# Kernel tuning notes

Hardware: AMD Instinct MI355X
Metric: run time of the kernel (lower is better)

## Reference

```python
import jax, jax.numpy as jnp
import numpy as np

N = 50000    # nodes
E = 600000   # edges
H = 128      # hidden_dim
NF = 12      # n_features
L = 4        # n_layers
EPS = 1e-5   # LayerNorm eps


def setup_inputs() -> dict:
    key = jax.random.key(0)
    ks = jax.random.split(key, 32)

    def w(k, shape, fan_in):
        return (jax.random.normal(k, shape, jnp.float32) / np.float32(np.sqrt(fan_in)))

    inp = {
        "x": jax.random.normal(ks[0], (N, NF), jnp.float32),
        "edge_index": jax.random.randint(ks[1], (2, E), 0, N, dtype=jnp.int64),
        # encoder: Linear(NF,H) -> ReLU -> Linear(H,H)
        "enc_W1": w(ks[2], (NF, H), NF), "enc_b1": jnp.zeros((H,), jnp.float32),
        "enc_W2": w(ks[3], (H, H), H),   "enc_b2": jnp.zeros((H,), jnp.float32),
        # L residual SAGE blocks (PyG SAGEConv: lin_l on mean-aggr w/ bias, lin_r on self no bias)
        "lin_l_W": w(ks[4], (L, H, H), H), "lin_l_b": jnp.zeros((L, H), jnp.float32),
        "lin_r_W": w(ks[5], (L, H, H), H),
        "ln_g": jnp.ones((L, H), jnp.float32), "ln_b": jnp.zeros((L, H), jnp.float32),
        # disp head: H->H->H//2->3
        "dW1": w(ks[6], (H, H), H),      "db1": jnp.zeros((H,), jnp.float32),
        "dW2": w(ks[7], (H, H // 2), H), "db2": jnp.zeros((H // 2,), jnp.float32),
        "dW3": w(ks[8], (H // 2, 3), H // 2), "db3": jnp.zeros((3,), jnp.float32),
        # stress head: H->H->H//2->1
        "sW1": w(ks[9], (H, H), H),       "sb1": jnp.zeros((H,), jnp.float32),
        "sW2": w(ks[10], (H, H // 2), H), "sb2": jnp.zeros((H // 2,), jnp.float32),
        "sW3": w(ks[11], (H // 2, 1), H // 2), "sb3": jnp.zeros((1,), jnp.float32),
    }
    return inp


def reference(x, edge_index, enc_W1, enc_b1, enc_W2, enc_b2,
              lin_l_W, lin_l_b, lin_r_W, ln_g, ln_b,
              dW1, db1, dW2, db2, dW3, db3,
              sW1, sb1, sW2, sb2, sW3, sb3):
    src, dst = edge_index[0], edge_index[1]

    # linear load-scaling ratio from load columns [3:6]
    load_mag = jnp.linalg.norm(x[:, 3:6], axis=1)
    ratio = jnp.max(load_mag)

    # encoder MLP
    h = jnp.maximum(x @ enc_W1 + enc_b1, 0.0) @ enc_W2 + enc_b2  # [N, H]

    # in-degree for mean aggregation (clamped to 1 like PyG)
    deg = jax.ops.segment_sum(jnp.ones((E,), h.dtype), dst, num_segments=N)
    inv_deg = 1.0 / jnp.clip(deg, 1.0)[:, None]  # [N, 1]

    for l in range(L):
        # SAGEConv: mean of neighbor (src) features at dst, then lin_l(aggr) + lin_r(self)
        agg = jax.ops.segment_sum(h[src], dst, num_segments=N) * inv_deg  # [N, H]
        y = agg @ lin_l_W[l] + lin_l_b[l] + h @ lin_r_W[l]
        # LayerNorm over channels
        mu = jnp.mean(y, axis=-1, keepdims=True)
        var = jnp.var(y, axis=-1, keepdims=True)
        y = (y - mu) * jax.lax.rsqrt(var + EPS) * ln_g[l] + ln_b[l]
        # residual + ReLU
        h = h + jnp.maximum(y, 0.0)

    # heads
    d = jnp.maximum(h @ dW1 + db1, 0.0)
    d = jnp.maximum(d @ dW2 + db2, 0.0) @ dW3 + db3  # [N, 3]
    s = jnp.maximum(h @ sW1 + sb1, 0.0)
    s = jnp.maximum(s @ sW2 + sb2, 0.0) @ sW3 + sb3  # [N, 1]

    # linear_scaling = True
    d = d * ratio
    s = s * ratio
    return jnp.concatenate([d, s], axis=1)  # [N, 4]
```

## Files before the change

### kernel.cpp

```cpp
#include <hip/hip_runtime.h>
#include <hip/hip_bf16.h>

typedef __hip_bfloat16 bf16;
typedef short bf16x8 __attribute__((ext_vector_type(8)));
typedef float f32x4 __attribute__((ext_vector_type(4)));

#define CAP 40

__device__ __forceinline__ float2 bfpair(unsigned u){
  float2 r; r.x = __uint_as_float(u<<16); r.y = __uint_as_float(u & 0xffff0000u); return r;
}
__device__ __forceinline__ float bfu(unsigned short u){ return __uint_as_float(((unsigned)u)<<16); }
__device__ __forceinline__ unsigned f2bf(float f){
  unsigned u = __float_as_uint(f);
  return (u + 0x7fffu + ((u>>16)&1u)) >> 16;
}
__device__ __forceinline__ unsigned fpack(float a, float b){
  return (f2bf(b)<<16) | f2bf(a);
}
__device__ __forceinline__ int edge_is64(const int* e){
  return (e[1]==0) & (e[3]==0) & (e[5]==0);
}
__device__ __forceinline__ int edge_ld(const int* e, int is64, int idx){
  return e[is64 ? 2*idx : idx];
}

__global__ __launch_bounds__(256) void k_we2(const float* __restrict__ eW2,
                                             unsigned short* __restrict__ WE2){
  int idx = (int)blockIdx.x*256 + threadIdx.x;
  int j = idx & 7;
  int lane = (idx>>3) & 63;
  int q = lane >> 4, p = lane & 15;
  int nt = (idx>>9) & 7, ks = (idx>>12) & 3;
  int k = ks*32 + q*8 + j, n = nt*16 + p;
  WE2[idx] = (unsigned short)f2bf(eW2[(size_t)k*128 + n]);
}

__global__ __launch_bounds__(256) void k_mega(
  const float* __restrict__ x, const int* __restrict__ eidx,
  int* __restrict__ cnt, unsigned short* __restrict__ csr,
  const float* __restrict__ llW, const float* __restrict__ lrW,
  const float* __restrict__ dW1, const float* __restrict__ sW1,
  const float* __restrict__ dW2, const float* __restrict__ sW2,
  unsigned short* __restrict__ WTs, unsigned short* __restrict__ WT1,
  unsigned short* __restrict__ WT2, unsigned* __restrict__ ratio,
  const float* __restrict__ W1, const float* __restrict__ b1,
  const unsigned short* __restrict__ WE2, const float* __restrict__ b2,
  bf16* __restrict__ h, int N, int E, int nbS)
{
  int i = (int)blockIdx.x;
  bool isScat = ((i % 6) == 0) && ((i / 6) < nbS);
  if(isScat){
    int b = i / 6;
    int is64 = edge_is64(eidx);
    int ebase = b*2048 + threadIdx.x;
    int sv[8], dv[8], pv[8];
    bool vv[8];
    #pragma unroll
    for(int t=0;t<8;t++){
      int e = ebase + t*256;
      vv[t] = e < E;
      dv[t] = 0; sv[t] = 0;
      if(vv[t]){ dv[t] = edge_ld(eidx,is64,E+e); sv[t] = edge_ld(eidx,is64,e); }
      vv[t] = vv[t] && (unsigned)dv[t] < (unsigned)N;
      if((unsigned)sv[t] >= (unsigned)N) sv[t] = 0;
    }
    #pragma unroll
    for(int t=0;t<8;t++){ pv[t] = -1; if(vv[t]) pv[t] = atomicAdd(&cnt[dv[t]], 1); }
    #pragma unroll
    for(int t=0;t<8;t++){
      if(vv[t] && pv[t] < CAP) csr[(size_t)dv[t]*CAP + pv[t]] = (unsigned short)sv[t];
    }
    return;
  }
  int nsb = (i + 5) / 6; if(nsb > nbS) nsb = nbS;
  int f = i - nsb;
  if(f < 704){
    int idx = f*256 + threadIdx.x;
    int j = idx & 7;
    int lane = (idx>>3) & 63;
    int q = lane >> 4, p = lane & 15;
    if(idx < 131072){
      int nt = (idx>>9) & 7, ks = (idx>>12) & 7, l = (idx>>15) & 3;
      int k = ks*32 + q*8 + j, n = nt*16 + p;
      float v = (k<128) ? llW[(size_t)l*16384 + (size_t)k*128 + n]
                        : lrW[(size_t)l*16384 + (size_t)(k-128)*128 + n];
      WTs[idx] = (unsigned short)f2bf(v);
    } else if(idx < 163840){
      int i2 = idx - 131072;
      int nt = (i2>>9) & 15, ks = (i2>>13) & 3;
      int k = ks*32 + q*8 + j, n = nt*16 + p;
      float v = (n<128) ? dW1[(size_t)k*128 + n] : sW1[(size_t)k*128 + (n-128)];
      WT1[i2] = (unsigned short)f2bf(v);
    } else {
      int i2 = idx - 163840;
      int nt = (i2>>9) & 7, ks = (i2>>12) & 3;
      int k = ks*32 + q*8 + j, n = nt*16 + p;
      float v = (n<64) ? dW2[(size_t)k*64 + n] : sW2[(size_t)k*64 + (n-64)];
      WT2[i2] = (unsigned short)f2bf(v);
    }
    return;
  }
  if(f < 768){
    int idx = (f - 704)*256 + threadIdx.x;
    int stride = 64*256;
    float m = 0.f;
    for(; idx<N; idx+=stride){
      float a = x[(size_t)idx*12+3];
      float bb = x[(size_t)idx*12+4];
      float c = x[(size_t)idx*12+5];
      m = fmaxf(m, sqrtf(a*a+bb*bb+c*c));
    }
    #pragma unroll
    for(int off=1; off<64; off<<=1) m = fmaxf(m, __shfl_xor(m, off));
    if((threadIdx.x & 63)==0) atomicMax(ratio, __float_as_uint(m));
    return;
  }
  __shared__ float Xs[64][12];
  __shared__ float W1s[12][128];
  __shared__ float b1s[128];
  __shared__ __align__(16) unsigned short T1b[64][136];
  int tid = threadIdx.x;
  int tx = tid & 31, ty = tid >> 5;
  int rowBase = (f - 768)*64;
  for(int idx=tid; idx<768; idx+=256){
    int r = idx/12, c = idx - r*12;
    int row = rowBase + r;
    Xs[r][c] = (row<N)? x[(size_t)row*12+c] : 0.f;
  }
  for(int idx=tid; idx<1536; idx+=256) W1s[idx>>7][idx&127] = W1[idx];
  if(tid<128) b1s[tid] = b1[tid];
  __syncthreads();
  float acc[8][4] = {};
  #pragma unroll
  for(int k=0;k<12;k++){
    float4 w4 = *(float4*)&W1s[k][tx*4];
    #pragma unroll
    for(int r=0;r<8;r++){
      float a = Xs[ty*8+r][k];
      acc[r][0]+=a*w4.x; acc[r][1]+=a*w4.y; acc[r][2]+=a*w4.z; acc[r][3]+=a*w4.w;
    }
  }
  #pragma unroll
  for(int r=0;r<8;r++)
    #pragma unroll
    for(int c=0;c<4;c++)
      T1b[ty*8+r][tx*4+c] = (unsigned short)f2bf(fmaxf(acc[r][c] + b1s[tx*4+c], 0.f));
  __syncthreads();

  int lane = tid & 63;
  int w = tid >> 6, q = lane >> 4, p = lane & 15;
  f32x4 acc2[8];
  #pragma unroll
  for(int nt=0; nt<8; nt++) acc2[nt] = (f32x4){0.f,0.f,0.f,0.f};
  #pragma unroll
  for(int ks=0; ks<4; ks++){
    bf16x8 af = *(const bf16x8*)&T1b[w*16+p][ks*32+q*8];
    #pragma unroll
    for(int nt=0; nt<8; nt++){
      bf16x8 bfr = *(const bf16x8*)(WE2 + ((size_t)(ks*8+nt)*64 + lane)*8);
      acc2[nt] = __builtin_amdgcn_mfma_f32_16x16x32_bf16(af, bfr, acc2[nt], 0,0,0);
    }
  }
  float b2v[8];
  #pragma unroll
  for(int nt=0; nt<8; nt++) b2v[nt] = b2[nt*16+p];
  unsigned short* hu = (unsigned short*)h;
  #pragma unroll
  for(int r=0;r<4;r++){
    int row = rowBase + w*16 + q*4 + r;
    if(row < N){
      #pragma unroll
      for(int nt=0; nt<8; nt++)
        hu[(size_t)row*128 + nt*16+p] = (unsigned short)f2bf(acc2[nt][r] + b2v[nt]);
    }
  }
}

__global__ __launch_bounds__(256) void k_layer16(
    const bf16* __restrict__ hin, bf16* __restrict__ hout,
    const int* __restrict__ cnt, const unsigned short* __restrict__ csr,
    const unsigned short* __restrict__ WT,
    const float* __restrict__ bl, const float* __restrict__ lng,
    const float* __restrict__ lnb, int N)
{
  __shared__ __align__(16) unsigned short Ag[16][136];
  __shared__ float sPart[4][16];
  __shared__ float qPart[4][16];
  int tid = threadIdx.x;
  int rowBase = blockIdx.x*16;

  {
    int qw = tid >> 4;
    int l  = tid & 15;
    int grp16 = (qw & 3) * 16;
    int row = rowBase + qw;
    float a0=0.f,a1=0.f,a2=0.f,a3=0.f,a4=0.f,a5=0.f,a6=0.f,a7=0.f;
    int dc = 0;
    int i0 = 0, i1 = 0, i2 = 0;
    if(row < N){
      dc = cnt[row]; if(dc > CAP) dc = CAP;
      const unsigned short* cp = csr + (size_t)row*CAP;
      if(l      < dc) i0 = cp[l];
      if(l + 16 < dc) i1 = cp[l + 16];
      if(l + 32 < dc) i2 = cp[l + 32];
    }

    {
      uint4 u[16];
      int jv[16];
      #pragma unroll
      for(int t=0;t<16;t++) jv[t] = __shfl(i0, grp16 + t);
      #pragma unroll
      for(int t=0;t<16;t++){
        u[t] = (uint4){0u,0u,0u,0u};
        if(t < dc) u[t] = *(const uint4*)(hin + (size_t)jv[t]*128 + l*8);
      }
      #pragma unroll
      for(int t=0;t<16;t++){
        float2 f;
        f=bfpair(u[t].x); a0+=f.x; a1+=f.y;  f=bfpair(u[t].y); a2+=f.x; a3+=f.y;
        f=bfpair(u[t].z); a4+=f.x; a5+=f.y;  f=bfpair(u[t].w); a6+=f.x; a7+=f.y;
      }
    }
    for(int i=16; i<dc; i+=4){
      uint4 u[4];
      int jv[4];
      #pragma unroll
      for(int t=0;t<4;t++){
        int it = i + t;
        int rsel = (it < 32) ? i1 : i2;
        jv[t] = __shfl(rsel, grp16 + (it & 15));
      }
      #pragma unroll
      for(int t=0;t<4;t++){
        u[t] = (uint4){0u,0u,0u,0u};
        if(i + t < dc) u[t] = *(const uint4*)(hin + (size_t)jv[t]*128 + l*8);
      }
      #pragma unroll
      for(int t=0;t<4;t++){
        float2 f;
        f=bfpair(u[t].x); a0+=f.x; a1+=f.y;  f=bfpair(u[t].y); a2+=f.x; a3+=f.y;
        f=bfpair(u[t].z); a4+=f.x; a5+=f.y;  f=bfpair(u[t].w); a6+=f.x; a7+=f.y;
      }
    }
    float id = 1.0f / (float)(dc>0? dc : 1);
    a0*=id; a1*=id; a2*=id; a3*=id; a4*=id; a5*=id; a6*=id; a7*=id;

    uint4 o;
    o.x = fpack(a0,a1); o.y = fpack(a2,a3);
    o.z = fpack(a4,a5); o.w = fpack(a6,a7);
    *(uint4*)&Ag[qw][l*8] = o;
  }
  __syncthreads();

  int lane = tid & 63;
  int w = tid >> 6;
  int q = lane >> 4;
  int p = lane & 15;
  int nt0 = 2*w, nt1 = 2*w+1;
  int am = rowBase + p;
  bool ok = am < N;
  const unsigned short* hRow = (const unsigned short*)hin + (size_t)am*128;

  f32x4 accA = (f32x4){0.f,0.f,0.f,0.f};
  f32x4 accB = (f32x4){0.f,0.f,0.f,0.f};
  #pragma unroll
  for(int ks=0; ks<8; ks++){
    bf16x8 af;
    if(ks < 4){
      af = *(const bf16x8*)&Ag[p][ks*32 + q*8];
    } else {
      af = (bf16x8){0,0,0,0,0,0,0,0};
      if(ok) af = *(const bf16x8*)(hRow + (ks-4)*32 + q*8);
    }
    bf16x8 b0 = *(const bf16x8*)(WT + ((size_t)(ks*8+nt0)*64 + lane)*8);
    bf16x8 b1 = *(const bf16x8*)(WT + ((size_t)(ks*8+nt1)*64 + lane)*8);
    accA = __builtin_amdgcn_mfma_f32_16x16x32_bf16(af, b0, accA, 0,0,0);
    accB = __builtin_amdgcn_mfma_f32_16x16x32_bf16(af, b1, accB, 0,0,0);
  }

  int c0 = nt0*16 + p, c1 = nt1*16 + p;
  float bl0 = bl[c0], g0 = lng[c0], lb0 = lnb[c0];
  float bl1 = bl[c1], g1 = lng[c1], lb1 = lnb[c1];
  float y0[4], y1[4];
  #pragma unroll
  for(int r=0;r<4;r++){
    y0[r] = accA[r] + bl0;
    y1[r] = accB[r] + bl1;
    float s  = y0[r] + y1[r];
    float sq = y0[r]*y0[r] + y1[r]*y1[r];
    #pragma unroll
    for(int off=1; off<16; off<<=1){ s += __shfl_xor(s, off); sq += __shfl_xor(sq, off); }
    if(p==0){ sPart[w][q*4+r] = s; qPart[w][q*4+r] = sq; }
  }
  __syncthreads();

  const unsigned short* hiu = (const unsigned short*)hin;
  unsigned short* hou = (unsigned short*)hout;
  #pragma unroll
  for(int r=0;r<4;r++){
    int rloc = q*4 + r;
    float s  = sPart[0][rloc]+sPart[1][rloc]+sPart[2][rloc]+sPart[3][rloc];
    float sq = qPart[0][rloc]+qPart[1][rloc]+qPart[2][rloc]+qPart[3][rloc];
    float mu = s*(1.f/128.f);
    float var = fmaxf(sq*(1.f/128.f) - mu*mu, 0.f);
    float rstd = rsqrtf(var + 1e-5f);
    int row = rowBase + rloc;
    if(row < N){
      float h0 = bfu(hiu[(size_t)row*128 + c0]);
      float h1 = bfu(hiu[(size_t)row*128 + c1]);
      float o0 = h0 + fmaxf((y0[r]-mu)*rstd*g0 + lb0, 0.f);
      float o1 = h1 + fmaxf((y1[r]-mu)*rstd*g1 + lb1, 0.f);
      hou[(size_t)row*128 + c0] = (unsigned short)f2bf(o0);
      hou[(size_t)row*128 + c1] = (unsigned short)f2bf(o1);
    }
  }
}

__global__ __launch_bounds__(256) void k_heads_mfma(
  const bf16* __restrict__ h,
  const unsigned short* __restrict__ WT1,
  const unsigned short* __restrict__ WT2,
  const float* __restrict__ db1, const float* __restrict__ sb1,
  const float* __restrict__ db2, const float* __restrict__ sb2,
  const float* __restrict__ dW3, const float* __restrict__ db3,
  const float* __restrict__ sW3, const float* __restrict__ sb3,
  const float* __restrict__ ratio_p, float* __restrict__ out, int N)
{
  __shared__ __align__(16) unsigned short T1s[4][16][264];
  const float ratio = *ratio_p;
  int tid = threadIdx.x;
  int lane = tid & 63;
  int w = tid >> 6;
  int q = lane >> 4;
  int p = lane & 15;
  int rowBase = blockIdx.x*64;
  int am = rowBase + w*16 + p;
  bool arow_ok = am < N;
  const unsigned short* hRow = (const unsigned short*)h + (size_t)am*128;

  f32x4 acc1[16];
  #pragma unroll
  for(int nt=0; nt<16; nt++) acc1[nt] = (f32x4){0.f,0.f,0.f,0.f};
  #pragma unroll
  for(int ks=0; ks<4; ks++){
    int koff = ks*32 + q*8;
    bf16x8 af = {0,0,0,0,0,0,0,0};
    if(arow_ok) af = *(const bf16x8*)(hRow + koff);
    #pragma unroll
    for(int nt=0; nt<16; nt++){
      bf16x8 bfr = *(const bf16x8*)(WT1 + ((size_t)(ks*16+nt)*64 + lane)*8);
      acc1[nt] = __builtin_amdgcn_mfma_f32_16x16x32_bf16(af, bfr, acc1[nt], 0,0,0);
    }
  }
  #pragma unroll
  for(int nt=0; nt<16; nt++){
    float b1v = (nt<8) ? db1[nt*16+p] : sb1[(nt-8)*16+p];
    #pragma unroll
    for(int r=0;r<4;r++){
      float v = fmaxf(acc1[nt][r] + b1v, 0.f);
      T1s[w][q*4+r][nt*16+p] = (unsigned short)f2bf(v);
    }
  }
  __syncthreads();

  f32x4 acc2[8];
  #pragma unroll
  for(int nt=0; nt<8; nt++) acc2[nt] = (f32x4){0.f,0.f,0.f,0.f};
  #pragma unroll
  for(int ks=0; ks<4; ks++){
    int koff = ks*32 + q*8;
    bf16x8 ad = *(const bf16x8*)&T1s[w][p][koff];
    bf16x8 as = *(const bf16x8*)&T1s[w][p][128+koff];
    #pragma unroll
    for(int nt=0; nt<8; nt++){
      bf16x8 bfr = *(const bf16x8*)(WT2 + ((size_t)(ks*8+nt)*64 + lane)*8);
      acc2[nt] = __builtin_amdgcn_mfma_f32_16x16x32_bf16(nt<4? ad : as, bfr, acc2[nt], 0,0,0);
    }
  }

  float w3d[4][3], w3s[4], bd2[4], bs2[4];
  #pragma unroll
  for(int nt=0; nt<4; nt++){
    #pragma unroll
    for(int c=0;c<3;c++) w3d[nt][c] = dW3[(nt*16+p)*3 + c];
    w3s[nt] = sW3[nt*16+p];
    bd2[nt] = db2[nt*16+p];
    bs2[nt] = sb2[nt*16+p];
  }
  float b3v = (p==0)? db3[0] : (p==1)? db3[1] : (p==2)? db3[2] : sb3[0];
  #pragma unroll
  for(int r=0;r<4;r++){
    int row = rowBase + w*16 + q*4 + r;
    float pd0=0.f, pd1=0.f, pd2=0.f, ps=0.f;
    #pragma unroll
    for(int nt=0; nt<4; nt++){
      float td = fmaxf(acc2[nt][r]   + bd2[nt], 0.f);
      float ts = fmaxf(acc2[nt+4][r] + bs2[nt], 0.f);
      pd0 += td*w3d[nt][0]; pd1 += td*w3d[nt][1]; pd2 += td*w3d[nt][2];
      ps  += ts*w3s[nt];
    }
    #pragma unroll
    for(int off=1; off<16; off<<=1){
      pd0 += __shfl_xor(pd0, off); pd1 += __shfl_xor(pd1, off);
      pd2 += __shfl_xor(pd2, off); ps  += __shfl_xor(ps, off);
    }
    if(row < N && p < 4){
      float v = (p==0)? pd0 : (p==1)? pd1 : (p==2)? pd2 : ps;
      out[(size_t)row*4 + p] = (v + b3v)*ratio;
    }
  }
}

extern "C" void kernel_launch(void* const* d_in, const int* in_sizes, int n_in,
                              void* d_out, int out_size, void* d_ws, size_t ws_size,
                              hipStream_t stream)
{
  const float* x   = (const float*)d_in[0];
  const int*  eidx = (const int*) d_in[1];
  const float* eW1 = (const float*)d_in[2];
  const float* eb1 = (const float*)d_in[3];
  const float* eW2 = (const float*)d_in[4];
  const float* eb2 = (const float*)d_in[5];
  const float* llW = (const float*)d_in[6];
  const float* llb = (const float*)d_in[7];
  const float* lrW = (const float*)d_in[8];
  const float* lng = (const float*)d_in[9];
  const float* lnb = (const float*)d_in[10];
  const float* dW1 = (const float*)d_in[11];
  const float* db1 = (const float*)d_in[12];
  const float* dW2 = (const float*)d_in[13];
  const float* db2 = (const float*)d_in[14];
  const float* dW3 = (const float*)d_in[15];
  const float* db3 = (const float*)d_in[16];
  const float* sW1 = (const float*)d_in[17];
  const float* sb1 = (const float*)d_in[18];
  const float* sW2 = (const float*)d_in[19];
  const float* sb2 = (const float*)d_in[20];
  const float* sW3 = (const float*)d_in[21];
  const float* sb3 = (const float*)d_in[22];
  float* out = (float*)d_out;

  const int N = in_sizes[0] / 12;
  const int E = in_sizes[1] / 2;
  (void)n_in; (void)out_size; (void)ws_size;

  char* base = (char*)d_ws;
  size_t off = 0;
  auto alloc = [&](size_t nbytes)->char*{
    char* p = base + off; off += (nbytes + 255) & ~(size_t)255; return p;
  };
  unsigned* ratio = (unsigned*)alloc(4);
  int*   cnt    = (int*)  alloc((size_t)N*4);
  unsigned short* csr = (unsigned short*)alloc((size_t)N*CAP*2);
  bf16*  hA     = (bf16*) alloc((size_t)N*128*2);
  bf16*  hB     = (bf16*) alloc((size_t)N*128*2);
  unsigned short* WTs  = (unsigned short*)alloc((size_t)131072*2);
  unsigned short* WT1h = (unsigned short*)alloc((size_t)32768*2);
  unsigned short* WT2h = (unsigned short*)alloc((size_t)16384*2);
  unsigned short* WE2  = (unsigned short*)alloc((size_t)16384*2);

  size_t zbytes = (size_t)((char*)csr - base);
  hipMemsetAsync(d_ws, 0, zbytes, stream);

  int nbS    = (E + 2047)/2048;
  int nbTile = (N + 63)/64;
  int nbLay  = (N + 15)/16;
  int nbF    = 768 + nbTile;

  k_we2 <<<64, 256, 0, stream>>>(eW2, WE2);
  k_mega<<<nbS + nbF, 256, 0, stream>>>(x, eidx, cnt, csr,
      llW, lrW, dW1, sW1, dW2, sW2, WTs, WT1h, WT2h, ratio,
      eW1, eb1, WE2, eb2, hA, N, E, nbS);

  bf16* hin = hA; bf16* hout = hB;
  for(int l=0;l<4;l++){
    k_layer16<<<nbLay, 256, 0, stream>>>(hin, hout, cnt, csr,
        WTs + (size_t)l*32768,
        llb + (size_t)l*128, lng + (size_t)l*128, lnb + (size_t)l*128, N);
    bf16* t = hin; hin = hout; hout = t;
  }
  k_heads_mfma<<<nbTile, 256, 0, stream>>>(hin, WT1h, WT2h,
      db1, sb1, db2, sb2, dW3, db3, sW3, sb3, (const float*)ratio, out, N);
}
```

Baseline: 321.9 us.

## Fuse last SAGE layer with output heads into one kernel

The fourth SAGE layer and both MLP heads now run in a single kernel, so the final hidden state stays in shared memory instead of being written to global memory and read back by a separate heads kernel. This drops one launch and one full N×128 bf16 round trip. The trade-off is that the heads now work on 16-row tiles spread across four waves, which needs more block-level syncs and cross-wave partial reductions, and the extra shared memory may lower occupancy. The gather code is moved into a shared device helper.

Result: faster. 315.3 us (median of 2 runs) (-2.1%).

```diff
diff --git a/kernel.cpp b/kernel.cpp
--- a/kernel.cpp
+++ b/kernel.cpp
@@ -49,11 +49,12 @@
   bf16* __restrict__ h, int N, int E, int nbS)
 {
   int i = (int)blockIdx.x;
+  int tid = threadIdx.x;
   bool isScat = ((i % 6) == 0) && ((i / 6) < nbS);
   if(isScat){
     int b = i / 6;
     int is64 = edge_is64(eidx);
-    int ebase = b*2048 + threadIdx.x;
+    int ebase = b*2048 + tid;
     int sv[8], dv[8], pv[8];
     bool vv[8];
     #pragma unroll
@@ -76,7 +77,7 @@
   int nsb = (i + 5) / 6; if(nsb > nbS) nsb = nbS;
   int f = i - nsb;
   if(f < 704){
-    int idx = f*256 + threadIdx.x;
+    int idx = f*256 + tid;
     int j = idx & 7;
     int lane = (idx>>3) & 63;
     int q = lane >> 4, p = lane & 15;
@@ -102,7 +103,7 @@
     return;
   }
   if(f < 768){
-    int idx = (f - 704)*256 + threadIdx.x;
+    int idx = (f - 704)*256 + tid;
     int stride = 64*256;
     float m = 0.f;
     for(; idx<N; idx+=stride){
@@ -113,14 +114,13 @@
     }
     #pragma unroll
     for(int off=1; off<64; off<<=1) m = fmaxf(m, __shfl_xor(m, off));
-    if((threadIdx.x & 63)==0) atomicMax(ratio, __float_as_uint(m));
+    if((tid & 63)==0) atomicMax(ratio, __float_as_uint(m));
     return;
   }
   __shared__ float Xs[64][12];
   __shared__ float W1s[12][128];
   __shared__ float b1s[128];
   __shared__ __align__(16) unsigned short T1b[64][136];
-  int tid = threadIdx.x;
   int tx = tid & 31, ty = tid >> 5;
   int rowBase = (f - 768)*64;
   for(int idx=tid; idx<768; idx+=256){
@@ -175,6 +175,71 @@
         hu[(size_t)row*128 + nt*16+p] = (unsigned short)f2bf(acc2[nt][r] + b2v[nt]);
     }
   }
+}
+
+__device__ __forceinline__ void gather_phase(int tid, int rowBase,
+    const bf16* __restrict__ hin, const int* __restrict__ cnt,
+    const unsigned short* __restrict__ csr, int N,
+    unsigned short (&Ag)[16][136])
+{
+  int qw = tid >> 4;
+  int l  = tid & 15;
+  int grp16 = (qw & 3) * 16;
+  int row = rowBase + qw;
+  float a0=0.f,a1=0.f,a2=0.f,a3=0.f,a4=0.f,a5=0.f,a6=0.f,a7=0.f;
+  int dc = 0;
+  int i0 = 0, i1 = 0, i2 = 0;
+  if(row < N){
+    dc = cnt[row]; if(dc > CAP) dc = CAP;
+    const unsigned short* cp = csr + (size_t)row*CAP;
+    if(l      < dc) i0 = cp[l];
+    if(l + 16 < dc) i1 = cp[l + 16];
+    if(l + 32 < dc) i2 = cp[l + 32];
+  }
+  {
+    uint4 u[16];
+    int jv[16];
+    #pragma unroll
+    for(int t=0;t<16;t++) jv[t] = __shfl(i0, grp16 + t);
+    #pragma unroll
+    for(int t=0;t<16;t++){
+      u[t] = (uint4){0u,0u,0u,0u};
+      if(t < dc) u[t] = *(const uint4*)(hin + (size_t)jv[t]*128 + l*8);
+    }
+    #pragma unroll
+    for(int t=0;t<16;t++){
+      float2 f;
+      f=bfpair(u[t].x); a0+=f.x; a1+=f.y;  f=bfpair(u[t].y); a2+=f.x; a3+=f.y;
+      f=bfpair(u[t].z); a4+=f.x; a5+=f.y;  f=bfpair(u[t].w); a6+=f.x; a7+=f.y;
+    }
+  }
+  for(int i=16; i<dc; i+=4){
+    uint4 u[4];
+    int jv[4];
+    #pragma unroll
+    for(int t=0;t<4;t++){
+      int it = i + t;
+      int rsel = (it < 32) ? i1 : i2;
+      jv[t] = __shfl(rsel, grp16 + (it & 15));
+    }
+    #pragma unroll
+    for(int t=0;t<4;t++){
+      u[t] = (uint4){0u,0u,0u,0u};
+      if(i + t < dc) u[t] = *(const uint4*)(hin + (size_t)jv[t]*128 + l*8);
+    }
+    #pragma unroll
+    for(int t=0;t<4;t++){
+      float2 f;
+      f=bfpair(u[t].x); a0+=f.x; a1+=f.y;  f=bfpair(u[t].y); a2+=f.x; a3+=f.y;
+      f=bfpair(u[t].z); a4+=f.x; a5+=f.y;  f=bfpair(u[t].w); a6+=f.x; a7+=f.y;
+    }
+  }
+  float id = 1.0f / (float)(dc>0? dc : 1);
+  a0*=id; a1*=id; a2*=id; a3*=id; a4*=id; a5*=id; a6*=id; a7*=id;
+  uint4 o;
+  o.x = fpack(a0,a1); o.y = fpack(a2,a3);
+  o.z = fpack(a4,a5); o.w = fpack(a6,a7);
+  *(uint4*)&Ag[qw][l*8] = o;
 }
 
 __global__ __launch_bounds__(256) void k_layer16(
@@ -190,68 +255,7 @@
   int tid = threadIdx.x;
   int rowBase = blockIdx.x*16;
 
-  {
-    int qw = tid >> 4;
-    int l  = tid & 15;
-    int grp16 = (qw & 3) * 16;
-    int row = rowBase + qw;
-    float a0=0.f,a1=0.f,a2=0.f,a3=0.f,a4=0.f,a5=0.f,a6=0.f,a7=0.f;
-    int dc = 0;
-    int i0 = 0, i1 = 0, i2 = 0;
-    if(row < N){
-      dc = cnt[row]; if(dc > CAP) dc = CAP;
-      const unsigned short* cp = csr + (size_t)row*CAP;
-      if(l      < dc) i0 = cp[l];
-      if(l + 16 < dc) i1 = cp[l + 16];
-      if(l + 32 < dc) i2 = cp[l + 32];
-    }
-
-    {
-      uint4 u[16];
-      int jv[16];
-      #pragma unroll
-      for(int t=0;t<16;t++) jv[t] = __shfl(i0, grp16 + t);
-      #pragma unroll
-      for(int t=0;t<16;t++){
-        u[t] = (uint4){0u,0u,0u,0u};
-        if(t < dc) u[t] = *(const uint4*)(hin + (size_t)jv[t]*128 + l*8);
-      }
-      #pragma unroll
-      for(int t=0;t<16;t++){
-        float2 f;
-        f=bfpair(u[t].x); a0+=f.x; a1+=f.y;  f=bfpair(u[t].y); a2+=f.x; a3+=f.y;
-        f=bfpair(u[t].z); a4+=f.x; a5+=f.y;  f=bfpair(u[t].w); a6+=f.x; a7+=f.y;
-      }
-    }
-    for(int i=16; i<dc; i+=4){
-      uint4 u[4];
-      int jv[4];
-      #pragma unroll
-      for(int t=0;t<4;t++){
-        int it = i + t;
-        int rsel = (it < 32) ? i1 : i2;
-        jv[t] = __shfl(rsel, grp16 + (it & 15));
-      }
-      #pragma unroll
-      for(int t=0;t<4;t++){
-        u[t] = (uint4){0u,0u,0u,0u};
-        if(i + t < dc) u[t] = *(const uint4*)(hin + (size_t)jv[t]*128 + l*8);
-      }
-      #pragma unroll
-      for(int t=0;t<4;t++){
-        float2 f;
-        f=bfpair(u[t].x); a0+=f.x; a1+=f.y;  f=bfpair(u[t].y); a2+=f.x; a3+=f.y;
-        f=bfpair(u[t].z); a4+=f.x; a5+=f.y;  f=bfpair(u[t].w); a6+=f.x; a7+=f.y;
-      }
-    }
-    float id = 1.0f / (float)(dc>0? dc : 1);
-    a0*=id; a1*=id; a2*=id; a3*=id; a4*=id; a5*=id; a6*=id; a7*=id;
-
-    uint4 o;
-    o.x = fpack(a0,a1); o.y = fpack(a2,a3);
-    o.z = fpack(a4,a5); o.w = fpack(a6,a7);
-    *(uint4*)&Ag[qw][l*8] = o;
-  }
+  gather_phase(tid, rowBase, hin, cnt, csr, N, Ag);
   __syncthreads();
 
   int lane = tid & 63;
@@ -318,97 +322,189 @@
   }
 }
 
-__global__ __launch_bounds__(256) void k_heads_mfma(
-  const bf16* __restrict__ h,
-  const unsigned short* __restrict__ WT1,
-  const unsigned short* __restrict__ WT2,
-  const float* __restrict__ db1, const float* __restrict__ sb1,
-  const float* __restrict__ db2, const float* __restrict__ sb2,
-  const float* __restrict__ dW3, const float* __restrict__ db3,
-  const float* __restrict__ sW3, const float* __restrict__ sb3,
-  const float* __restrict__ ratio_p, float* __restrict__ out, int N)
+__global__ __launch_bounds__(256) void k_layer16h(
+    const bf16* __restrict__ hin,
+    const int* __restrict__ cnt, const unsigned short* __restrict__ csr,
+    const unsigned short* __restrict__ WT,
+    const float* __restrict__ bl, const float* __restrict__ lng,
+    const float* __restrict__ lnb,
+    const unsigned short* __restrict__ WT1,
+    const unsigned short* __restrict__ WT2,
+    const float* __restrict__ db1, const float* __restrict__ sb1,
+    const float* __restrict__ db2, const float* __restrict__ sb2,
+    const float* __restrict__ dW3, const float* __restrict__ db3,
+    const float* __restrict__ sW3, const float* __restrict__ sb3,
+    const float* __restrict__ ratio_p, float* __restrict__ out, int N)
 {
-  __shared__ __align__(16) unsigned short T1s[4][16][264];
-  const float ratio = *ratio_p;
+  __shared__ __align__(16) unsigned short Ag[16][136];
+  __shared__ float sPart[4][16];
+  __shared__ float qPart[4][16];
+  __shared__ __align__(16) unsigned short h4[16][136];
+  __shared__ __align__(16) unsigned short T1[16][264];
+  __shared__ float partD[2][16][3];
+  __shared__ float partS[2][16];
   int tid = threadIdx.x;
+  int rowBase = blockIdx.x*16;
+
+  gather_phase(tid, rowBase, hin, cnt, csr, N, Ag);
+  __syncthreads();
+
   int lane = tid & 63;
   int w = tid >> 6;
   int q = lane >> 4;
   int p = lane & 15;
-  int rowBase = blockIdx.x*64;
-  int am = rowBase + w*16 + p;
-  bool arow_ok = am < N;
-  const unsigned short* hRow = (const unsigned short*)h + (size_t)am*128;
-
-  f32x4 acc1[16];
-  #pragma unroll
-  for(int nt=0; nt<16; nt++) acc1[nt] = (f32x4){0.f,0.f,0.f,0.f};
-  #pragma unroll
-  for(int ks=0; ks<4; ks++){
-    int koff = ks*32 + q*8;
-    bf16x8 af = {0,0,0,0,0,0,0,0};
-    if(arow_ok) af = *(const bf16x8*)(hRow + koff);
-    #pragma unroll
-    for(int nt=0; nt<16; nt++){
-      bf16x8 bfr = *(const bf16x8*)(WT1 + ((size_t)(ks*16+nt)*64 + lane)*8);
-      acc1[nt] = __builtin_amdgcn_mfma_f32_16x16x32_bf16(af, bfr, acc1[nt], 0,0,0);
-    }
-  }
-  #pragma unroll
-  for(int nt=0; nt<16; nt++){
-    float b1v = (nt<8) ? db1[nt*16+p] : sb1[(nt-8)*16+p];
+  int nt0 = 2*w, nt1 = 2*w+1;
+  int am = rowBase + p;
+  bool ok = am < N;
+  const unsigned short* hRow = (const unsigned short*)hin + (size_t)am*128;
+
+  f32x4 accA = (f32x4){0.f,0.f,0.f,0.f};
+  f32x4 accB = (f32x4){0.f,0.f,0.f,0.f};
+  #pragma unroll
+  for(int ks=0; ks<8; ks++){
+    bf16x8 af;
+    if(ks < 4){
+      af = *(const bf16x8*)&Ag[p][ks*32 + q*8];
+    } else {
+      af = (bf16x8){0,0,0,0,0,0,0,0};
+      if(ok) af = *(const bf16x8*)(hRow + (ks-4)*32 + q*8);
+    }
+    bf16x8 b0 = *(const bf16x8*)(WT + ((size_t)(ks*8+nt0)*64 + lane)*8);
+    bf16x8 b1 = *(const bf16x8*)(WT + ((size_t)(ks*8+nt1)*64 + lane)*8);
+    accA = __builtin_amdgcn_mfma_f32_16x16x32_bf16(af, b0, accA, 0,0,0);
+    accB = __builtin_amdgcn_mfma_f32_16x16x32_bf16(af, b1, accB, 0,0,0);
+  }
+
+  int c0 = nt0*16 + p, c1 = nt1*16 + p;
+  float bl0 = bl[c0], g0 = lng[c0], lb0 = lnb[c0];
+  float bl1 = bl[c1], g1 = lng[c1], lb1 = lnb[c1];
+  float y0[4], y1[4];
+  #pragma unroll
+  for(int r=0;r<4;r++){
+    y0[r] = accA[r] + bl0;
+    y1[r] = accB[r] + bl1;
+    float s  = y0[r] + y1[r];
+    float sq = y0[r]*y0[r] + y1[r]*y1[r];
+    #pragma unroll
+    for(int off=1; off<16; off<<=1){ s += __shfl_xor(s, off); sq += __shfl_xor(sq, off); }
+    if(p==0){ sPart[w][q*4+r] = s; qPart[w][q*4+r] = sq; }
+  }
+  __syncthreads();
+
+  const unsigned short* hiu = (const unsigned short*)hin;
+  #pragma unroll
+  for(int r=0;r<4;r++){
+    int rloc = q*4 + r;
+    float s  = sPart[0][rloc]+sPart[1][rloc]+sPart[2][rloc]+sPart[3][rloc];
+    float sq = qPart[0][rloc]+qPart[1][rloc]+qPart[2][rloc]+qPart[3][rloc];
+    float mu = s*(1.f/128.f);
+    float var = fmaxf(sq*(1.f/128.f) - mu*mu, 0.f);
+    float rstd = rsqrtf(var + 1e-5f);
+    int row = rowBase + rloc;
+    unsigned short v0 = 0, v1 = 0;
+    if(row < N){
+      float h0 = bfu(hiu[(size_t)row*128 + c0]);
+      float h1 = bfu(hiu[(size_t)row*128 + c1]);
+      v0 = (unsigned short)f2bf(h0 + fmaxf((y0[r]-mu)*rstd*g0 + lb0, 0.f));
+      v1 = (unsigned short)f2bf(h1 + fmaxf((y1[r]-mu)*rstd*g1 + lb1, 0.f));
+    }
+    h4[rloc][c0] = v0;
+    h4[rloc][c1] = v1;
+  }
+  __syncthreads();
+
+  {
+    f32x4 acc1[4];
+    #pragma unroll
+    for(int j=0;j<4;j++) acc1[j] = (f32x4){0.f,0.f,0.f,0.f};
+    #pragma unroll
+    for(int ks=0; ks<4; ks++){
+      bf16x8 af = *(const bf16x8*)&h4[p][ks*32 + q*8];
+      #pragma unroll
+      for(int j=0;j<4;j++){
+        int nt = w*4 + j;
+        bf16x8 bfr = *(const bf16x8*)(WT1 + ((size_t)(ks*16+nt)*64 + lane)*8);
+        acc1[j] = __builtin_amdgcn_mfma_f32_16x16x32_bf16(af, bfr, acc1[j], 0,0,0);
+      }
+    }
+    #pragma unroll
+    for(int j=0;j<4;j++){
+      int nt = w*4 + j;
+      float b1v = (nt<8) ? db1[nt*16+p] : sb1[(nt-8)*16+p];
+      #pragma unroll
+      for(int r=0;r<4;r++){
+        float v = fmaxf(acc1[j][r] + b1v, 0.f);
+        T1[q*4+r][nt*16+p] = (unsigned short)f2bf(v);
+      }
+    }
+  }
+  __syncthreads();
+
+  {
+    bool isS = (w >= 2);
+    float pd0[4]={0,0,0,0}, pd1[4]={0,0,0,0}, pd2[4]={0,0,0,0}, ps[4]={0,0,0,0};
+    #pragma unroll
+    for(int jj=0; jj<2; jj++){
+      int nt2 = 2*w + jj;
+      f32x4 acc2 = (f32x4){0.f,0.f,0.f,0.f};
+      int abase = (nt2 < 4) ? 0 : 128;
+      #pragma unroll
+      for(int ks=0; ks<4; ks++){
+        bf16x8 a2 = *(const bf16x8*)&T1[p][abase + ks*32 + q*8];
+        bf16x8 bfr = *(const bf16x8*)(WT2 + ((size_t)(ks*8+nt2)*64 + lane)*8);
+        acc2 = __builtin_amdgcn_mfma_f32_16x16x32_bf16(a2, bfr, acc2, 0,0,0);
+      }
+      int jcol = (nt2 & 3)*16 + p;
+      if(!isS){
+        float b2v = db2[jcol];
+        float w30 = dW3[jcol*3+0], w31 = dW3[jcol*3+1], w32 = dW3[jcol*3+2];
+        #pragma unroll
+        for(int r=0;r<4;r++){
+          float td = fmaxf(acc2[r] + b2v, 0.f);
+          pd0[r] += td*w30; pd1[r] += td*w31; pd2[r] += td*w32;
+        }
+      } else {
+        float b2v = sb2[jcol];
+        float w3 = sW3[jcol];
+        #pragma unroll
+        for(int r=0;r<4;r++){
+          float ts = fmaxf(acc2[r] + b2v, 0.f);
+          ps[r] += ts*w3;
+        }
+      }
+    }
     #pragma unroll
     for(int r=0;r<4;r++){
-      float v = fmaxf(acc1[nt][r] + b1v, 0.f);
-      T1s[w][q*4+r][nt*16+p] = (unsigned short)f2bf(v);
-    }
-  }
-  __syncthreads();
-
-  f32x4 acc2[8];
-  #pragma unroll
-  for(int nt=0; nt<8; nt++) acc2[nt] = (f32x4){0.f,0.f,0.f,0.f};
-  #pragma unroll
-  for(int ks=0; ks<4; ks++){
-    int koff = ks*32 + q*8;
-    bf16x8 ad = *(const bf16x8*)&T1s[w][p][koff];
-    bf16x8 as = *(const bf16x8*)&T1s[w][p][128+koff];
-    #pragma unroll
-    for(int nt=0; nt<8; nt++){
-      bf16x8 bfr = *(const bf16x8*)(WT2 + ((size_t)(ks*8+nt)*64 + lane)*8);
-      acc2[nt] = __builtin_amdgcn_mfma_f32_16x16x32_bf16(nt<4? ad : as, bfr, acc2[nt], 0,0,0);
-    }
-  }
-
-  float w3d[4][3], w3s[4], bd2[4], bs2[4];
-  #pragma unroll
-  for(int nt=0; nt<4; nt++){
-    #pragma unroll
-    for(int c=0;c<3;c++) w3d[nt][c] = dW3[(nt*16+p)*3 + c];
-    w3s[nt] = sW3[nt*16+p];
-    bd2[nt] = db2[nt*16+p];
-    bs2[nt] = sb2[nt*16+p];
-  }
-  float b3v = (p==0)? db3[0] : (p==1)? db3[1] : (p==2)? db3[2] : sb3[0];
-  #pragma unroll
-  for(int r=0;r<4;r++){
-    int row = rowBase + w*16 + q*4 + r;
-    float pd0=0.f, pd1=0.f, pd2=0.f, ps=0.f;
-    #pragma unroll
-    for(int nt=0; nt<4; nt++){
-      float td = fmaxf(acc2[nt][r]   + bd2[nt], 0.f);
-      float ts = fmaxf(acc2[nt+4][r] + bs2[nt], 0.f);
-      pd0 += td*w3d[nt][0]; pd1 += td*w3d[nt][1]; pd2 += td*w3d[nt][2];
-      ps  += ts*w3s[nt];
-    }
-    #pragma unroll
-    for(int off=1; off<16; off<<=1){
-      pd0 += __shfl_xor(pd0, off); pd1 += __shfl_xor(pd1, off);
-      pd2 += __shfl_xor(pd2, off); ps  += __shfl_xor(ps, off);
-    }
-    if(row < N && p < 4){
-      float v = (p==0)? pd0 : (p==1)? pd1 : (p==2)? pd2 : ps;
-      out[(size_t)row*4 + p] = (v + b3v)*ratio;
+      #pragma unroll
+      for(int off=1; off<16; off<<=1){
+        pd0[r] += __shfl_xor(pd0[r], off);
+        pd1[r] += __shfl_xor(pd1[r], off);
+        pd2[r] += __shfl_xor(pd2[r], off);
+        ps[r]  += __shfl_xor(ps[r],  off);
+      }
+      if(p==0){
+        int rloc = q*4 + r;
+        if(!isS){
+          partD[w][rloc][0] = pd0[r];
+          partD[w][rloc][1] = pd1[r];
+          partD[w][rloc][2] = pd2[r];
+        } else {
+          partS[w-2][rloc] = ps[r];
+        }
+      }
+    }
+  }
+  __syncthreads();
+
+  if(tid < 64){
+    float ratioV = *ratio_p;
+    int rr = tid >> 2, comp = tid & 3;
+    int row = rowBase + rr;
+    if(row < N){
+      float v, b3;
+      if(comp < 3){ v = partD[0][rr][comp] + partD[1][rr][comp]; b3 = db3[comp]; }
+      else        { v = partS[0][rr] + partS[1][rr];             b3 = sb3[0]; }
+      out[(size_t)row*4 + comp] = (v + b3)*ratioV;
     }
   }
 }
@@ -475,12 +571,15 @@
       eW1, eb1, WE2, eb2, hA, N, E, nbS);
 
   bf16* hin = hA; bf16* hout = hB;
-  for(int l=0;l<4;l++){
+  for(int l=0;l<3;l++){
     k_layer16<<<nbLay, 256, 0, stream>>>(hin, hout, cnt, csr,
         WTs + (size_t)l*32768,
         llb + (size_t)l*128, lng + (size_t)l*128, lnb + (size_t)l*128, N);
     bf16* t = hin; hin = hout; hout = t;
   }
-  k_heads_mfma<<<nbTile, 256, 0, stream>>>(hin, WT1h, WT2h,
-      db1, sb1, db2, sb2, dW3, db3, sW3, sb3, (const float*)ratio, out, N);
-}
+  k_layer16h<<<nbLay, 256, 0, stream>>>(hin, cnt, csr,
+      WTs + (size_t)3*32768,
+      llb + (size_t)3*128, lng + (size_t)3*128, lnb + (size_t)3*128,
+      WT1h, WT2h, db1, sb1, db2, sb2, dW3, db3, sW3, sb3,
+      (const float*)ratio, out, N);
+}
```
